# Performance work log

Measured on AMD Instinct MI355X. Metric: run time of the kernel, lower is better.

## Reference

```python
import jax, jax.numpy as jnp
import numpy as np
from math import sqrt

HEADS = 16
DIM_HEAD = 64
EPS = 1e-4
MP_T = 0.3


def l2norm(t, eps=EPS):
    n = jnp.linalg.norm(t, axis=-1, keepdims=True)
    return t / jnp.maximum(n, eps)


def mp_linear(x, w):
    # weight-normalized linear: l2norm rows / sqrt(fan_in)
    fan_in = w.shape[1]
    wn = l2norm(w) / sqrt(fan_in)
    return x @ wn.T


def setup_inputs() -> dict:
    key = jax.random.key(0)
    k1, k2, k3, k4 = jax.random.split(key, 4)
    b, n, dim = 2, 2048, 1024
    x = jax.random.normal(k1, (b, n, dim), dtype=jnp.float32)
    w_qkv = jax.random.normal(k2, (3 * HEADS * DIM_HEAD, dim), dtype=jnp.float32)
    w_out = jax.random.normal(k3, (dim, HEADS * DIM_HEAD), dtype=jnp.float32)
    mem_kv = jax.random.normal(k4, (2, HEADS, 4, DIM_HEAD), dtype=jnp.float32)
    return {"x": x, "w_qkv": w_qkv, "w_out": w_out, "mem_kv": mem_kv}


def reference(x, w_qkv, w_out, mem_kv):
    b, n, dim = x.shape
    h, d = HEADS, DIM_HEAD
    scale = d ** -0.5

    qkv = mp_linear(x, w_qkv)                      # [b, n, 3*h*d]
    q, k, v = jnp.split(qkv, 3, axis=-1)
    split_heads = lambda t: t.reshape(b, n, h, d).transpose(0, 2, 1, 3)  # b h n d
    q, k, v = map(split_heads, (q, k, v))

    mk = jnp.broadcast_to(mem_kv[0], (b, h, mem_kv.shape[2], d))
    mv = jnp.broadcast_to(mem_kv[1], (b, h, mem_kv.shape[2], d))
    k = jnp.concatenate([mk, k], axis=2)
    v = jnp.concatenate([mv, v], axis=2)

    # pixel_norm: l2 normalize over head dim, rescale by sqrt(d)
    pn = lambda t: l2norm(t) * sqrt(d)
    q, k, v = pn(q), pn(k), pn(v)

    q = q * scale
    sim = jnp.einsum('bhid,bhjd->bhij', q, k)
    attn = jax.nn.softmax(sim, axis=-1)
    out = jnp.einsum('bhij,bhjd->bhid', attn, v)
    out = out.transpose(0, 2, 1, 3).reshape(b, n, h * d)
    out = mp_linear(out, w_out)

    # magnitude-preserving residual add
    t = MP_T
    return (out * (1.0 - t) + x * t) / sqrt((1.0 - t) ** 2 + t ** 2)
```

## Files before the change

### kernel.cpp

```cpp
#include <hip/hip_runtime.h>
#include <hip/hip_bf16.h>
#include <math.h>


#define EPSN 1e-4f
#define NKEY 2112
#define LOG2E 1.4426950408889634f

typedef __attribute__((ext_vector_type(8))) short short8;
typedef __attribute__((ext_vector_type(4))) short short4v;
typedef __attribute__((ext_vector_type(4))) float floatx4;

typedef __attribute__((address_space(1))) const void g_void;
typedef __attribute__((address_space(3))) void lds_void;

__device__ __forceinline__ void async16(void* lds, const void* g) {
    __builtin_amdgcn_global_load_lds((g_void*)g, (lds_void*)lds, 16, 0, 0);
}

__device__ __forceinline__ short f2bf(float f) {
    union { float f; unsigned u; } c{f};
    unsigned r = (c.u + 0x7FFF + ((c.u >> 16) & 1)) >> 16;
    return (short)r;
}
__device__ __forceinline__ short f2bf_fast(float f) {
    union { float f; unsigned u; } c{f};
    return (short)((c.u + 0x8000) >> 16);
}

__global__ __launch_bounds__(256) void prep_inputs(const float* __restrict__ x,
                                                   const float* __restrict__ w_qkv,
                                                   const float* __restrict__ w_out,
                                                   const float* __restrict__ memkv,
                                                   short* __restrict__ xb,
                                                   short* __restrict__ wnqkv,
                                                   short* __restrict__ wnout,
                                                   short* __restrict__ Kb,
                                                   short* __restrict__ Vt) {
    const int bid = blockIdx.x, tid = threadIdx.x;
    if (bid < 4096) {
        int i = bid * 1024 + tid * 4;
        float4 v = *(const float4*)(x + i);
        short4v s = {f2bf(v.x), f2bf(v.y), f2bf(v.z), f2bf(v.w)};
        *(short4v*)(xb + i) = s;
        return;
    }
    if (bid < 8192) {
        const float* w; short* wn; int r;
        if (bid < 7168) { w = w_qkv; wn = wnqkv; r = bid - 4096; }
        else            { w = w_out; wn = wnout; r = bid - 7168; }
        __shared__ float red[256];
        const float* row = w + (size_t)r * 1024;
        float ss = 0.f;
        for (int c = tid; c < 1024; c += 256) { float v = row[c]; ss += v * v; }
        red[tid] = ss;
        __syncthreads();
        for (int s = 128; s > 0; s >>= 1) {
            if (tid < s) red[tid] += red[tid + s];
            __syncthreads();
        }
        float f = 1.0f / (fmaxf(sqrtf(red[0]), EPSN) * 32.0f);
        for (int c = tid; c < 1024; c += 256) wn[(size_t)r * 1024 + c] = f2bf(row[c] * f);
        return;
    }
    const int bh = bid - 8192, h = bh & 15;
    const int r = tid >> 2, part = tid & 3;
    if (r < 4) {
        const float* pk = memkv + (size_t)(h * 4 + r) * 64 + part * 16;
        const float* pv = memkv + (size_t)((16 + h) * 4 + r) * 64 + part * 16;
        float k[16], v[16]; float ssk = 0.f, ssv = 0.f;
        #pragma unroll
        for (int i = 0; i < 16; i += 4) {
            float4 a = *(const float4*)(pk + i);
            float4 b = *(const float4*)(pv + i);
            k[i]=a.x; k[i+1]=a.y; k[i+2]=a.z; k[i+3]=a.w;
            v[i]=b.x; v[i+1]=b.y; v[i+2]=b.z; v[i+3]=b.w;
            ssk += a.x*a.x + a.y*a.y + a.z*a.z + a.w*a.w;
            ssv += b.x*b.x + b.y*b.y + b.z*b.z + b.w*b.w;
        }
        ssk += __shfl_xor(ssk, 1); ssk += __shfl_xor(ssk, 2);
        ssv += __shfl_xor(ssv, 1); ssv += __shfl_xor(ssv, 2);
        const float fk = 8.0f / fmaxf(sqrtf(ssk), EPSN);
        const float fv = 8.0f / fmaxf(sqrtf(ssv), EPSN);
        short* kd = Kb + ((size_t)bh * NKEY + r) * 64 + part * 16;
        #pragma unroll
        for (int i = 0; i < 16; i++) kd[i] = f2bf(k[i] * fk);
        #pragma unroll
        for (int i = 0; i < 16; i++)
            Vt[((size_t)bh * 64 + part * 16 + i) * NKEY + r] = f2bf(v[i] * fv);
    }
    for (int p = tid; p < 480; p += 256)
        *(short8*)(Kb + ((size_t)bh * NKEY + 2052) * 64 + p * 8) = (short8){0,0,0,0,0,0,0,0};
    for (int p = tid; p < 960; p += 256) {
        int row = p / 15, c = p % 15;
        *(short4v*)(Vt + ((size_t)bh * 64 + row) * NKEY + 2052 + c * 4) = (short4v){0,0,0,0};
    }
}

__global__ __launch_bounds__(256) void gemm_qkv(const short* __restrict__ A,
                                                const short* __restrict__ B,
                                                short* __restrict__ Qb,
                                                short* __restrict__ Kb,
                                                short* __restrict__ Vt) {
    constexpr int K = 1024;
    __shared__ __align__(16) short As[2][128 * 32];
    __shared__ __align__(16) short Bs[2][128 * 32];
    const int tid = threadIdx.x;
    const int wv = tid >> 6, lane = tid & 63;
    const int l16 = lane & 15, quad = lane >> 4;
    const int wr = wv >> 1, wc = wv & 1;
    const int bm0 = blockIdx.y * 128, bn0 = blockIdx.x * 128;
    const int grow = lane >> 2;
    const int gk = (lane & 3) * 8;

    floatx4 acc[4][4];
    #pragma unroll
    for (int i = 0; i < 4; i++)
        #pragma unroll
        for (int j = 0; j < 4; j++) acc[i][j] = (floatx4){0.f, 0.f, 0.f, 0.f};

    const short* Abase = A + (size_t)(bm0 + wv * 32 + grow) * K + gk;
    const short* Bbase = B + (size_t)(bn0 + wv * 32 + grow) * K + gk;

    #pragma unroll
    for (int j = 0; j < 2; j++) {
        async16(&As[0][(wv * 32 + j * 16) * 32], Abase + (size_t)(j * 16) * K);
        async16(&Bs[0][(wv * 32 + j * 16) * 32], Bbase + (size_t)(j * 16) * K);
    }
    const int NKI = K >> 5;
    for (int ki = 0; ki < NKI; ki++) {
        const int cur = ki & 1;
        if (ki + 1 < NKI) {
            const int nxt = cur ^ 1;
            const int off = (ki + 1) * 32;
            #pragma unroll
            for (int j = 0; j < 2; j++) {
                async16(&As[nxt][(wv * 32 + j * 16) * 32], Abase + (size_t)(j * 16) * K + off);
                async16(&Bs[nxt][(wv * 32 + j * 16) * 32], Bbase + (size_t)(j * 16) * K + off);
            }
            asm volatile("s_waitcnt vmcnt(4)" ::: "memory");
        } else {
            asm volatile("s_waitcnt vmcnt(0)" ::: "memory");
        }
        asm volatile("s_barrier" ::: "memory");
        short8 aA[4], bB[4];
        #pragma unroll
        for (int i = 0; i < 4; i++)
            aA[i] = *(const short8*)&As[cur][(wr * 64 + i * 16 + l16) * 32 + quad * 8];
        #pragma unroll
        for (int j = 0; j < 4; j++)
            bB[j] = *(const short8*)&Bs[cur][(wc * 64 + j * 16 + l16) * 32 + quad * 8];
        #pragma unroll
        for (int i = 0; i < 4; i++)
            #pragma unroll
            for (int j = 0; j < 4; j++)
                acc[i][j] = __builtin_amdgcn_mfma_f32_16x16x32_bf16(aA[i], bB[j], acc[i][j], 0, 0, 0);
        asm volatile("s_barrier" ::: "memory");
    }

    const int colbase = bn0 + wc * 64;
    const int which = colbase >> 10;
    const int h = (colbase >> 6) & 15;
    float sc[4][4];
    #pragma unroll
    for (int i = 0; i < 4; i++)
        #pragma unroll
        for (int r = 0; r < 4; r++) {
            float ss = 0.f;
            #pragma unroll
            for (int j = 0; j < 4; j++) ss += acc[i][j][r] * acc[i][j][r];
            ss += __shfl_xor(ss, 1); ss += __shfl_xor(ss, 2);
            ss += __shfl_xor(ss, 4); ss += __shfl_xor(ss, 8);
            const float num = (which == 0) ? LOG2E : 8.0f;
            sc[i][r] = num / fmaxf(sqrtf(ss), EPSN);
        }
    if (which == 2) {
        #pragma unroll
        for (int i = 0; i < 4; i++) {
            const int row0 = bm0 + wr * 64 + i * 16 + quad * 4;
            const int bh = (row0 >> 11) * 16 + h;
            const int tok0 = row0 & 2047;
            #pragma unroll
            for (int j = 0; j < 4; j++) {
                const int d = j * 16 + l16;
                short4v o = {f2bf(acc[i][j][0] * sc[i][0]), f2bf(acc[i][j][1] * sc[i][1]),
                             f2bf(acc[i][j][2] * sc[i][2]), f2bf(acc[i][j][3] * sc[i][3])};
                *(short4v*)(Vt + ((size_t)bh * 64 + d) * NKEY + 4 + tok0) = o;
            }
        }
    } else {
        #pragma unroll
        for (int i = 0; i < 4; i++)
            #pragma unroll
            for (int r = 0; r < 4; r++) {
                const int row = bm0 + wr * 64 + i * 16 + quad * 4 + r;
                const int bh = (row >> 11) * 16 + h;
                const int tok = row & 2047;
                const size_t base = (which == 0) ? ((size_t)bh * 2048 + tok) * 64
                                                 : ((size_t)bh * NKEY + 4 + tok) * 64;
                short* dst = (which == 0) ? Qb : Kb;
                #pragma unroll
                for (int j = 0; j < 4; j++)
                    dst[base + j * 16 + l16] = f2bf(acc[i][j][r] * sc[i][r]);
            }
    }
}

template<int MT, int NT>
__global__ __launch_bounds__(256) void gemm_mfma(const short* __restrict__ A,
                                                 const short* __restrict__ B,
                                                 float* __restrict__ C,
                                                 int M, int N, int K,
                                                 const float* __restrict__ resid) {
    constexpr int FI = MT / 32;
    constexpr int FJ = NT / 32;
    constexpr int nA = MT / 64;
    constexpr int nB = NT / 64;
    __shared__ __align__(16) short As[2][MT * 32];
    __shared__ __align__(16) short Bs[2][NT * 32];
    const int tid = threadIdx.x;
    const int wv = tid >> 6, lane = tid & 63;
    const int l16 = lane & 15, quad = lane >> 4;
    const int wr = wv >> 1, wc = wv & 1;
    const int bm0 = blockIdx.y * MT, bn0 = blockIdx.x * NT;
    const int grow = lane >> 2;
    const int gk = (lane & 3) * 8;

    floatx4 acc[FI][FJ];
    #pragma unroll
    for (int i = 0; i < FI; i++)
        #pragma unroll
        for (int j = 0; j < FJ; j++) acc[i][j] = (floatx4){0.f, 0.f, 0.f, 0.f};

    const short* Abase = A + (size_t)(bm0 + wv * (MT / 4) + grow) * K + gk;
    const short* Bbase = B + (size_t)(bn0 + wv * (NT / 4) + grow) * K + gk;

    #pragma unroll
    for (int j = 0; j < nA; j++)
        async16(&As[0][(wv * (MT / 4) + j * 16) * 32], Abase + (size_t)(j * 16) * K);
    #pragma unroll
    for (int j = 0; j < nB; j++)
        async16(&Bs[0][(wv * (NT / 4) + j * 16) * 32], Bbase + (size_t)(j * 16) * K);

    const int NKI = K >> 5;
    for (int ki = 0; ki < NKI; ki++) {
        const int cur = ki & 1;
        if (ki + 1 < NKI) {
            const int nxt = cur ^ 1;
            const int off = (ki + 1) * 32;
            #pragma unroll
            for (int j = 0; j < nA; j++)
                async16(&As[nxt][(wv * (MT / 4) + j * 16) * 32], Abase + (size_t)(j * 16) * K + off);
            #pragma unroll
            for (int j = 0; j < nB; j++)
                async16(&Bs[nxt][(wv * (NT / 4) + j * 16) * 32], Bbase + (size_t)(j * 16) * K + off);
            if constexpr (nA + nB == 4)      asm volatile("s_waitcnt vmcnt(4)" ::: "memory");
            else if constexpr (nA + nB == 3) asm volatile("s_waitcnt vmcnt(3)" ::: "memory");
            else                             asm volatile("s_waitcnt vmcnt(2)" ::: "memory");
        } else {
            asm volatile("s_waitcnt vmcnt(0)" ::: "memory");
        }
        asm volatile("s_barrier" ::: "memory");
        short8 aA[FI], bB[FJ];
        #pragma unroll
        for (int i = 0; i < FI; i++)
            aA[i] = *(const short8*)&As[cur][(wr * (MT / 2) + i * 16 + l16) * 32 + quad * 8];
        #pragma unroll
        for (int j = 0; j < FJ; j++)
            bB[j] = *(const short8*)&Bs[cur][(wc * (NT / 2) + j * 16 + l16) * 32 + quad * 8];
        #pragma unroll
        for (int i = 0; i < FI; i++)
            #pragma unroll
            for (int j = 0; j < FJ; j++)
                acc[i][j] = __builtin_amdgcn_mfma_f32_16x16x32_bf16(aA[i], bB[j], acc[i][j], 0, 0, 0);
        asm volatile("s_barrier" ::: "memory");
    }
    #pragma unroll
    for (int i = 0; i < FI; i++)
        #pragma unroll
        for (int j = 0; j < FJ; j++)
            #pragma unroll
            for (int r = 0; r < 4; r++) {
                const int row = bm0 + wr * (MT / 2) + i * 16 + quad * 4 + r;
                const int col = bn0 + wc * (NT / 2) + j * 16 + l16;
                const size_t idx = (size_t)row * N + col;
                float v = acc[i][j][r];
                if (resid) v = (v * 0.7f + resid[idx] * 0.3f) * 1.3130643285972254f;
                C[idx] = v;
            }
}

__global__ __launch_bounds__(256) void attn_mfma(const short* __restrict__ Qb,
                                                 const short* __restrict__ Kb,
                                                 const short* __restrict__ Vt,
                                                 short* __restrict__ out) {
    const int bh = blockIdx.x;
    const int q0 = blockIdx.y * 128;
    const int tid = threadIdx.x;
    const int wave = tid >> 6, lane = tid & 63;
    const int l16 = lane & 15, quad = lane >> 4;

    __shared__ __align__(16) short Ks2[2][2][64 * 32];
    __shared__ __align__(16) short Vs2[2][2][64 * 32];
    __shared__ __align__(16) short Pw[4][32 * 72];

    const short* qbase = Qb + ((size_t)bh * 2048 + q0 + wave * 32 + l16) * 64;
    short8 bQ[2][2];
    #pragma unroll
    for (int qg = 0; qg < 2; qg++)
        #pragma unroll
        for (int dh = 0; dh < 2; dh++)
            bQ[qg][dh] = *(const short8*)(qbase + qg * 1024 + dh * 32 + quad * 8);
    asm volatile("s_waitcnt vmcnt(0)" ::: "memory");

    const int grow = lane >> 2, gsub = (lane & 3) * 8;
    auto issue = [&](int tile, int buf) {
        #pragma unroll
        for (int s = 0; s < 4; s++) {
            const int u = wave * 4 + s;
            if (u < 8) {
                const int dh = u >> 2, kc = u & 3;
                async16(&Ks2[buf][dh][kc * 512],
                        Kb + ((size_t)bh * NKEY + tile * 64 + kc * 16 + grow) * 64 + dh * 32 + gsub);
            } else {
                const int v = u - 8;
                const int kh = v >> 2, dc = v & 3;
                async16(&Vs2[buf][kh][dc * 512],
                        Vt + ((size_t)bh * 64 + dc * 16 + grow) * NKEY + tile * 64 + kh * 32 + gsub);
            }
        }
    };

    floatx4 O[4][2];
    #pragma unroll
    for (int dt = 0; dt < 4; dt++)
        #pragma unroll
        for (int qg = 0; qg < 2; qg++) O[dt][qg] = (floatx4){0.f, 0.f, 0.f, 0.f};
    float lp[2] = {0.f, 0.f};

    issue(0, 0);
    for (int tile = 0; tile < 33; tile++) {
        const int cur = tile & 1;
        if (tile < 32) {
            issue(tile + 1, cur ^ 1);
            asm volatile("s_waitcnt vmcnt(4)" ::: "memory");
        } else {
            asm volatile("s_waitcnt vmcnt(0)" ::: "memory");
        }
        asm volatile("s_barrier" ::: "memory");

        floatx4 S[4][2];
        #pragma unroll
        for (int kt = 0; kt < 4; kt++) {
            short8 aK0 = *(const short8*)&Ks2[cur][0][(kt * 16 + l16) * 32 + quad * 8];
            short8 aK1 = *(const short8*)&Ks2[cur][1][(kt * 16 + l16) * 32 + quad * 8];
            #pragma unroll
            for (int qg = 0; qg < 2; qg++) {
                floatx4 s = (floatx4){-12.f, -12.f, -12.f, -12.f};
                s = __builtin_amdgcn_mfma_f32_16x16x32_bf16(aK0, bQ[qg][0], s, 0, 0, 0);
                s = __builtin_amdgcn_mfma_f32_16x16x32_bf16(aK1, bQ[qg][1], s, 0, 0, 0);
                S[kt][qg] = s;
            }
        }
        if (tile == 32) {
            #pragma unroll
            for (int kt = 0; kt < 4; kt++)
                #pragma unroll
                for (int qg = 0; qg < 2; qg++)
                    if (kt > 0 || quad > 0)
                        S[kt][qg] = (floatx4){-1e30f, -1e30f, -1e30f, -1e30f};
        }
        #pragma unroll
        for (int kt = 0; kt < 4; kt++)
            #pragma unroll
            for (int qg = 0; qg < 2; qg++) {
                float p0 = __builtin_amdgcn_exp2f(S[kt][qg][0]);
                float p1 = __builtin_amdgcn_exp2f(S[kt][qg][1]);
                float p2 = __builtin_amdgcn_exp2f(S[kt][qg][2]);
                float p3 = __builtin_amdgcn_exp2f(S[kt][qg][3]);
                lp[qg] += (p0 + p1) + (p2 + p3);
                short4v pk = {f2bf_fast(p0), f2bf_fast(p1), f2bf_fast(p2), f2bf_fast(p3)};
                *(short4v*)&Pw[wave][(qg * 16 + l16) * 72 + kt * 16 + quad * 4] = pk;
            }
        short8 bP[2][2];
        #pragma unroll
        for (int qg = 0; qg < 2; qg++)
            #pragma unroll
            for (int kh = 0; kh < 2; kh++)
                bP[qg][kh] = *(const short8*)&Pw[wave][(qg * 16 + l16) * 72 + kh * 32 + quad * 8];
        #pragma unroll
        for (int dt = 0; dt < 4; dt++) {
            short8 aV0 = *(const short8*)&Vs2[cur][0][(dt * 16 + l16) * 32 + quad * 8];
            short8 aV1 = *(const short8*)&Vs2[cur][1][(dt * 16 + l16) * 32 + quad * 8];
            #pragma unroll
            for (int qg = 0; qg < 2; qg++) {
                O[dt][qg] = __builtin_amdgcn_mfma_f32_16x16x32_bf16(aV0, bP[qg][0], O[dt][qg], 0, 0, 0);
                O[dt][qg] = __builtin_amdgcn_mfma_f32_16x16x32_bf16(aV1, bP[qg][1], O[dt][qg], 0, 0, 0);
            }
        }
        asm volatile("s_barrier" ::: "memory");
    }

    const int bb = bh >> 4, h = bh & 15;
    float inv[2];
    #pragma unroll
    for (int qg = 0; qg < 2; qg++) {
        float l = lp[qg];
        l += __shfl_xor(l, 16);
        l += __shfl_xor(l, 32);
        inv[qg] = 1.0f / l;
    }
    #pragma unroll
    for (int dt = 0; dt < 4; dt++)
        #pragma unroll
        for (int qg = 0; qg < 2; qg++) {
            const int token = q0 + wave * 32 + qg * 16 + l16;
            short4v o = {f2bf(O[dt][qg][0] * inv[qg]), f2bf(O[dt][qg][1] * inv[qg]),
                         f2bf(O[dt][qg][2] * inv[qg]), f2bf(O[dt][qg][3] * inv[qg])};
            *(short4v*)(out + ((size_t)(bb * 2048 + token)) * 1024 + h * 64 + dt * 16 + quad * 4) = o;
        }
}

extern "C" void kernel_launch(void* const* d_in, const int* in_sizes, int n_in,
                              void* d_out, int out_size, void* d_ws, size_t ws_size,
                              hipStream_t stream) {
    const float* x      = (const float*)d_in[0];
    const float* w_qkv  = (const float*)d_in[1];
    const float* w_out  = (const float*)d_in[2];
    const float* mem_kv = (const float*)d_in[3];
    float* out = (float*)d_out;

    char* ws = (char*)d_ws;
    short* wnqkv_b = (short*)(ws);
    short* wnout_b = (short*)(ws + (6u << 20));
    short* xb      = (short*)(ws + (8u << 20));
    short* Qb      = (short*)(ws + (16u << 20));
    short* Kb      = (short*)(ws + (24u << 20));
    short* Vt      = (short*)(ws + (33u << 20));
    short* attnb   = (short*)(ws + (42u << 20));

    prep_inputs<<<8224, 256, 0, stream>>>(x, w_qkv, w_out, mem_kv,
                                          xb, wnqkv_b, wnout_b, Kb, Vt);

    gemm_qkv<<<dim3(3072 / 128, 4096 / 128), 256, 0, stream>>>(
        xb, wnqkv_b, Qb, Kb, Vt);

    attn_mfma<<<dim3(32, 16), 256, 0, stream>>>(Qb, Kb, Vt, attnb);

    gemm_mfma<128, 64><<<dim3(1024 / 64, 4096 / 128), 256, 0, stream>>>(
        attnb, wnout_b, out, 4096, 1024, 1024, x);
}
```

Baseline: 212.5 us.

## Split attention over key tiles across two blocks with a separate reduce kernel

Splits the 33 key tiles of attention into two halves handled by separate blocks (grid z=2), doubling the block count from 512 to 1024 to better fill the GPU's compute units. Each split writes unnormalized fp32 partial outputs and row sums to workspace, and a new reduce kernel sums the two, normalizes and converts to bf16. The max-free softmax with a fixed offset lets partials be added directly. It adds about 32MB of fp32 partial writes and reads plus an extra kernel launch.

After: 229.4 us. 8.0% more time.

```diff
diff --git a/kernel.cpp b/kernel.cpp
--- a/kernel.cpp
+++ b/kernel.cpp
@@ -293,9 +293,13 @@
 __global__ __launch_bounds__(256) void attn_mfma(const short* __restrict__ Qb,
                                                  const short* __restrict__ Kb,
                                                  const short* __restrict__ Vt,
-                                                 short* __restrict__ out) {
+                                                 float* __restrict__ Opart,
+                                                 float* __restrict__ lpart) {
     const int bh = blockIdx.x;
     const int q0 = blockIdx.y * 128;
+    const int split = blockIdx.z;
+    const int t0 = split * 17;
+    const int t1 = (t0 + 17 < 33) ? t0 + 17 : 33;
     const int tid = threadIdx.x;
     const int wave = tid >> 6, lane = tid & 63;
     const int l16 = lane & 15, quad = lane >> 4;
@@ -338,10 +342,10 @@
         for (int qg = 0; qg < 2; qg++) O[dt][qg] = (floatx4){0.f, 0.f, 0.f, 0.f};
     float lp[2] = {0.f, 0.f};
 
-    issue(0, 0);
-    for (int tile = 0; tile < 33; tile++) {
-        const int cur = tile & 1;
-        if (tile < 32) {
+    issue(t0, 0);
+    for (int tile = t0; tile < t1; tile++) {
+        const int cur = (tile - t0) & 1;
+        if (tile + 1 < t1) {
             issue(tile + 1, cur ^ 1);
             asm volatile("s_waitcnt vmcnt(4)" ::: "memory");
         } else {
@@ -402,23 +406,39 @@
     }
 
     const int bb = bh >> 4, h = bh & 15;
-    float inv[2];
     #pragma unroll
     for (int qg = 0; qg < 2; qg++) {
         float l = lp[qg];
         l += __shfl_xor(l, 16);
         l += __shfl_xor(l, 32);
-        inv[qg] = 1.0f / l;
-    }
-    #pragma unroll
-    for (int dt = 0; dt < 4; dt++)
-        #pragma unroll
-        for (int qg = 0; qg < 2; qg++) {
-            const int token = q0 + wave * 32 + qg * 16 + l16;
-            short4v o = {f2bf(O[dt][qg][0] * inv[qg]), f2bf(O[dt][qg][1] * inv[qg]),
-                         f2bf(O[dt][qg][2] * inv[qg]), f2bf(O[dt][qg][3] * inv[qg])};
-            *(short4v*)(out + ((size_t)(bb * 2048 + token)) * 1024 + h * 64 + dt * 16 + quad * 4) = o;
-        }
+        const int token = q0 + wave * 32 + qg * 16 + l16;
+        if (quad == 0)
+            lpart[((size_t)split * 32 + bh) * 2048 + token] = l;
+        #pragma unroll
+        for (int dt = 0; dt < 4; dt++) {
+            float4 o = {O[dt][qg][0], O[dt][qg][1], O[dt][qg][2], O[dt][qg][3]};
+            *(float4*)(Opart + (size_t)split * 4194304 +
+                       ((size_t)(bb * 2048 + token)) * 1024 + h * 64 + dt * 16 + quad * 4) = o;
+        }
+    }
+}
+
+__global__ __launch_bounds__(256) void reduce_attn(const float* __restrict__ Opart,
+                                                   const float* __restrict__ lpart,
+                                                   short* __restrict__ attnb) {
+    const int row = blockIdx.x;
+    const int col = threadIdx.x * 4;
+    const int bh = (row >> 11) * 16 + (col >> 6);
+    const int tok = row & 2047;
+    const float l0 = lpart[(size_t)bh * 2048 + tok];
+    const float l1 = lpart[(size_t)(32 + bh) * 2048 + tok];
+    const float inv = 1.0f / (l0 + l1);
+    const size_t idx = (size_t)row * 1024 + col;
+    float4 a = *(const float4*)(Opart + idx);
+    float4 b = *(const float4*)(Opart + 4194304 + idx);
+    short4v o = {f2bf((a.x + b.x) * inv), f2bf((a.y + b.y) * inv),
+                 f2bf((a.z + b.z) * inv), f2bf((a.w + b.w) * inv)};
+    *(short4v*)(attnb + idx) = o;
 }
 
 extern "C" void kernel_launch(void* const* d_in, const int* in_sizes, int n_in,
@@ -438,6 +458,8 @@
     short* Kb      = (short*)(ws + (24u << 20));
     short* Vt      = (short*)(ws + (33u << 20));
     short* attnb   = (short*)(ws + (42u << 20));
+    float* Opart   = (float*)(ws + (50u << 20));
+    float* lpart   = (float*)(ws + (82u << 20));
 
     prep_inputs<<<8224, 256, 0, stream>>>(x, w_qkv, w_out, mem_kv,
                                           xb, wnqkv_b, wnout_b, Kb, Vt);
@@ -445,7 +467,9 @@
     gemm_qkv<<<dim3(3072 / 128, 4096 / 128), 256, 0, stream>>>(
         xb, wnqkv_b, Qb, Kb, Vt);
 
-    attn_mfma<<<dim3(32, 16), 256, 0, stream>>>(Qb, Kb, Vt, attnb);
+    attn_mfma<<<dim3(32, 16, 2), 256, 0, stream>>>(Qb, Kb, Vt, Opart, lpart);
+
+    reduce_attn<<<4096, 256, 0, stream>>>(Opart, lpart, attnb);
 
     gemm_mfma<128, 64><<<dim3(1024 / 64, 4096 / 128), 256, 0, stream>>>(
         attnb, wnout_b, out, 4096, 1024, 1024, x);
```

## Restructure attention into single-wave blocks loading K/V directly from global

Applied to the files above, without the earlier changes.

Rewrites the attention kernel so each 64-thread block (one wave) handles 64 queries, loading K and V fragments directly from global memory into registers instead of staging them through double-buffered LDS with barriers. The grid doubles along the query axis. This removes the block barriers and LDS staging, and each wave reuses its K/V fragments across four query groups. In exchange, every wave fetches K/V from global/L2 itself with no cross-wave sharing, register pressure rises, and there is no explicit prefetch to hide load latency.

Result: slower. 229.2 us (+7.9%).

```diff
diff --git a/kernel.cpp b/kernel.cpp
--- a/kernel.cpp
+++ b/kernel.cpp
@@ -290,135 +290,96 @@
             }
 }
 
-__global__ __launch_bounds__(256) void attn_mfma(const short* __restrict__ Qb,
-                                                 const short* __restrict__ Kb,
-                                                 const short* __restrict__ Vt,
-                                                 short* __restrict__ out) {
+__global__ __launch_bounds__(64) void attn_mfma(const short* __restrict__ Qb,
+                                                const short* __restrict__ Kb,
+                                                const short* __restrict__ Vt,
+                                                short* __restrict__ attnb) {
     const int bh = blockIdx.x;
-    const int q0 = blockIdx.y * 128;
-    const int tid = threadIdx.x;
-    const int wave = tid >> 6, lane = tid & 63;
+    const int q0 = blockIdx.y * 64;
+    const int lane = threadIdx.x;
     const int l16 = lane & 15, quad = lane >> 4;
 
-    __shared__ __align__(16) short Ks2[2][2][64 * 32];
-    __shared__ __align__(16) short Vs2[2][2][64 * 32];
-    __shared__ __align__(16) short Pw[4][32 * 72];
-
-    const short* qbase = Qb + ((size_t)bh * 2048 + q0 + wave * 32 + l16) * 64;
-    short8 bQ[2][2];
-    #pragma unroll
-    for (int qg = 0; qg < 2; qg++)
+    __shared__ __align__(16) short Pw[64 * 72];
+
+    const short* qbase = Qb + ((size_t)bh * 2048 + q0 + l16) * 64;
+    short8 bQ[4][2];
+    #pragma unroll
+    for (int qg = 0; qg < 4; qg++)
         #pragma unroll
         for (int dh = 0; dh < 2; dh++)
-            bQ[qg][dh] = *(const short8*)(qbase + qg * 1024 + dh * 32 + quad * 8);
-    asm volatile("s_waitcnt vmcnt(0)" ::: "memory");
-
-    const int grow = lane >> 2, gsub = (lane & 3) * 8;
-    auto issue = [&](int tile, int buf) {
-        #pragma unroll
-        for (int s = 0; s < 4; s++) {
-            const int u = wave * 4 + s;
-            if (u < 8) {
-                const int dh = u >> 2, kc = u & 3;
-                async16(&Ks2[buf][dh][kc * 512],
-                        Kb + ((size_t)bh * NKEY + tile * 64 + kc * 16 + grow) * 64 + dh * 32 + gsub);
-            } else {
-                const int v = u - 8;
-                const int kh = v >> 2, dc = v & 3;
-                async16(&Vs2[buf][kh][dc * 512],
-                        Vt + ((size_t)bh * 64 + dc * 16 + grow) * NKEY + tile * 64 + kh * 32 + gsub);
-            }
-        }
-    };
-
-    floatx4 O[4][2];
+            bQ[qg][dh] = *(const short8*)(qbase + qg * 16 * 64 + dh * 32 + quad * 8);
+
+    floatx4 O[4][4];
     #pragma unroll
     for (int dt = 0; dt < 4; dt++)
         #pragma unroll
-        for (int qg = 0; qg < 2; qg++) O[dt][qg] = (floatx4){0.f, 0.f, 0.f, 0.f};
-    float lp[2] = {0.f, 0.f};
-
-    issue(0, 0);
+        for (int qg = 0; qg < 4; qg++) O[dt][qg] = (floatx4){0.f, 0.f, 0.f, 0.f};
+    float lp[4] = {0.f, 0.f, 0.f, 0.f};
+
+    const short* kb = Kb + (size_t)bh * NKEY * 64;
+    const short* vb = Vt + (size_t)bh * 64 * NKEY;
+
     for (int tile = 0; tile < 33; tile++) {
-        const int cur = tile & 1;
-        if (tile < 32) {
-            issue(tile + 1, cur ^ 1);
-            asm volatile("s_waitcnt vmcnt(4)" ::: "memory");
-        } else {
-            asm volatile("s_waitcnt vmcnt(0)" ::: "memory");
-        }
-        asm volatile("s_barrier" ::: "memory");
-
-        floatx4 S[4][2];
+        short8 aK[4][2], aV[4][2];
+        #pragma unroll
+        for (int kt = 0; kt < 4; kt++)
+            #pragma unroll
+            for (int dh = 0; dh < 2; dh++)
+                aK[kt][dh] = *(const short8*)(kb + ((size_t)(tile * 64 + kt * 16 + l16)) * 64 + dh * 32 + quad * 8);
+        #pragma unroll
+        for (int dt = 0; dt < 4; dt++)
+            #pragma unroll
+            for (int kh = 0; kh < 2; kh++)
+                aV[dt][kh] = *(const short8*)(vb + ((size_t)(dt * 16 + l16)) * NKEY + tile * 64 + kh * 32 + quad * 8);
+
         #pragma unroll
         for (int kt = 0; kt < 4; kt++) {
-            short8 aK0 = *(const short8*)&Ks2[cur][0][(kt * 16 + l16) * 32 + quad * 8];
-            short8 aK1 = *(const short8*)&Ks2[cur][1][(kt * 16 + l16) * 32 + quad * 8];
-            #pragma unroll
-            for (int qg = 0; qg < 2; qg++) {
+            #pragma unroll
+            for (int qg = 0; qg < 4; qg++) {
                 floatx4 s = (floatx4){-12.f, -12.f, -12.f, -12.f};
-                s = __builtin_amdgcn_mfma_f32_16x16x32_bf16(aK0, bQ[qg][0], s, 0, 0, 0);
-                s = __builtin_amdgcn_mfma_f32_16x16x32_bf16(aK1, bQ[qg][1], s, 0, 0, 0);
-                S[kt][qg] = s;
-            }
-        }
-        if (tile == 32) {
-            #pragma unroll
-            for (int kt = 0; kt < 4; kt++)
-                #pragma unroll
-                for (int qg = 0; qg < 2; qg++)
-                    if (kt > 0 || quad > 0)
-                        S[kt][qg] = (floatx4){-1e30f, -1e30f, -1e30f, -1e30f};
-        }
-        #pragma unroll
-        for (int kt = 0; kt < 4; kt++)
-            #pragma unroll
-            for (int qg = 0; qg < 2; qg++) {
-                float p0 = __builtin_amdgcn_exp2f(S[kt][qg][0]);
-                float p1 = __builtin_amdgcn_exp2f(S[kt][qg][1]);
-                float p2 = __builtin_amdgcn_exp2f(S[kt][qg][2]);
-                float p3 = __builtin_amdgcn_exp2f(S[kt][qg][3]);
+                s = __builtin_amdgcn_mfma_f32_16x16x32_bf16(aK[kt][0], bQ[qg][0], s, 0, 0, 0);
+                s = __builtin_amdgcn_mfma_f32_16x16x32_bf16(aK[kt][1], bQ[qg][1], s, 0, 0, 0);
+                if (tile == 32 && (kt > 0 || quad > 0))
+                    s = (floatx4){-1e30f, -1e30f, -1e30f, -1e30f};
+                float p0 = __builtin_amdgcn_exp2f(s[0]);
+                float p1 = __builtin_amdgcn_exp2f(s[1]);
+                float p2 = __builtin_amdgcn_exp2f(s[2]);
+                float p3 = __builtin_amdgcn_exp2f(s[3]);
                 lp[qg] += (p0 + p1) + (p2 + p3);
                 short4v pk = {f2bf_fast(p0), f2bf_fast(p1), f2bf_fast(p2), f2bf_fast(p3)};
-                *(short4v*)&Pw[wave][(qg * 16 + l16) * 72 + kt * 16 + quad * 4] = pk;
-            }
-        short8 bP[2][2];
-        #pragma unroll
-        for (int qg = 0; qg < 2; qg++)
+                *(short4v*)&Pw[(qg * 16 + l16) * 72 + kt * 16 + quad * 4] = pk;
+            }
+        }
+        short8 bP[4][2];
+        #pragma unroll
+        for (int qg = 0; qg < 4; qg++)
             #pragma unroll
             for (int kh = 0; kh < 2; kh++)
-                bP[qg][kh] = *(const short8*)&Pw[wave][(qg * 16 + l16) * 72 + kh * 32 + quad * 8];
-        #pragma unroll
-        for (int dt = 0; dt < 4; dt++) {
-            short8 aV0 = *(const short8*)&Vs2[cur][0][(dt * 16 + l16) * 32 + quad * 8];
-            short8 aV1 = *(const short8*)&Vs2[cur][1][(dt * 16 + l16) * 32 + quad * 8];
-            #pragma unroll
-            for (int qg = 0; qg < 2; qg++) {
-                O[dt][qg] = __builtin_amdgcn_mfma_f32_16x16x32_bf16(aV0, bP[qg][0], O[dt][qg], 0, 0, 0);
-                O[dt][qg] = __builtin_amdgcn_mfma_f32_16x16x32_bf16(aV1, bP[qg][1], O[dt][qg], 0, 0, 0);
-            }
-        }
-        asm volatile("s_barrier" ::: "memory");
+                bP[qg][kh] = *(const short8*)&Pw[(qg * 16 + l16) * 72 + kh * 32 + quad * 8];
+        #pragma unroll
+        for (int dt = 0; dt < 4; dt++)
+            #pragma unroll
+            for (int qg = 0; qg < 4; qg++) {
+                O[dt][qg] = __builtin_amdgcn_mfma_f32_16x16x32_bf16(aV[dt][0], bP[qg][0], O[dt][qg], 0, 0, 0);
+                O[dt][qg] = __builtin_amdgcn_mfma_f32_16x16x32_bf16(aV[dt][1], bP[qg][1], O[dt][qg], 0, 0, 0);
+            }
     }
 
     const int bb = bh >> 4, h = bh & 15;
-    float inv[2];
-    #pragma unroll
-    for (int qg = 0; qg < 2; qg++) {
+    #pragma unroll
+    for (int qg = 0; qg < 4; qg++) {
         float l = lp[qg];
         l += __shfl_xor(l, 16);
         l += __shfl_xor(l, 32);
-        inv[qg] = 1.0f / l;
-    }
-    #pragma unroll
-    for (int dt = 0; dt < 4; dt++)
-        #pragma unroll
-        for (int qg = 0; qg < 2; qg++) {
-            const int token = q0 + wave * 32 + qg * 16 + l16;
-            short4v o = {f2bf(O[dt][qg][0] * inv[qg]), f2bf(O[dt][qg][1] * inv[qg]),
-                         f2bf(O[dt][qg][2] * inv[qg]), f2bf(O[dt][qg][3] * inv[qg])};
-            *(short4v*)(out + ((size_t)(bb * 2048 + token)) * 1024 + h * 64 + dt * 16 + quad * 4) = o;
-        }
+        const float inv = 1.0f / l;
+        const int token = q0 + qg * 16 + l16;
+        #pragma unroll
+        for (int dt = 0; dt < 4; dt++) {
+            short4v o = {f2bf(O[dt][qg][0] * inv), f2bf(O[dt][qg][1] * inv),
+                         f2bf(O[dt][qg][2] * inv), f2bf(O[dt][qg][3] * inv)};
+            *(short4v*)(attnb + ((size_t)(bb * 2048 + token)) * 1024 + h * 64 + dt * 16 + quad * 4) = o;
+        }
+    }
 }
 
 extern "C" void kernel_launch(void* const* d_in, const int* in_sizes, int n_in,
@@ -445,7 +406,7 @@
     gemm_qkv<<<dim3(3072 / 128, 4096 / 128), 256, 0, stream>>>(
         xb, wnqkv_b, Qb, Kb, Vt);
 
-    attn_mfma<<<dim3(32, 16), 256, 0, stream>>>(Qb, Kb, Vt, attnb);
+    attn_mfma<<<dim3(32, 32), 64, 0, stream>>>(Qb, Kb, Vt, attnb);
 
     gemm_mfma<128, 64><<<dim3(1024 / 64, 4096 / 128), 256, 0, stream>>>(
         attnb, wnout_b, out, 4096, 1024, 1024, x);
```
